# Performance work log

Measured on AMD Instinct MI355X. Metric: run time of the kernel, lower is better.

## Reference

```python
import jax, jax.numpy as jnp
import numpy as np
from jax import lax

B, L, H = 2, 4096, 2048
NH = 16
DK = H // NH  # num_slot = 128 (q/k dim)
C = 64        # chunk size
EPS = 1e-5
N_LAYER = 24


def setup_inputs() -> dict:
    key = jax.random.key(0)
    ks = jax.random.split(key, 7)
    std = 0.02
    return {
        "hidden_states": jax.random.normal(ks[0], (B, L, H), jnp.float32),
        "Wq": jax.random.normal(ks[1], (DK, H), jnp.float32) * std,
        "Wk": jax.random.normal(ks[2], (DK, H), jnp.float32) * std,
        "Wog": jax.random.normal(ks[3], (H, H), jnp.float32) * std,
        "Wig": jax.random.normal(ks[4], (H, H), jnp.float32) * std,
        "Wo": jax.random.normal(ks[5], (H, H), jnp.float32) * (std / np.sqrt(2 * N_LAYER)),
        "g_norm_w": jnp.ones((H,), jnp.float32),
    }


def _gla_chunk(q, k, v, gf):
    # q,k,gf: [b,L,dk]; v: [b,L,dv]. Recurrence: S_t = diag(exp(gf_t)) S_{t-1} + k_t v_t^T; o_t = q_t S_t
    b, Ls, dk = q.shape
    dv = v.shape[-1]
    n = Ls // C
    # [n, b, C, d] so scan iterates over chunks
    qc = q.reshape(b, n, C, dk).transpose(1, 0, 2, 3)
    kc = k.reshape(b, n, C, dk).transpose(1, 0, 2, 3)
    vc = v.reshape(b, n, C, dv).transpose(1, 0, 2, 3)
    gc = gf.reshape(b, n, C, dk).transpose(1, 0, 2, 3)
    Bc = jnp.cumsum(gc, axis=2)  # inclusive within-chunk log-decay

    tril = jnp.tril(jnp.ones((C, C), bool))

    def step(S, inp):
        qh, kh, vh, Bh = inp  # [b,C,dk],[b,C,dk],[b,C,dv],[b,C,dk]
        Blast = Bh[:, -1, :]  # [b,dk]
        # exp(B_i - B_j) <= 1 for j <= i (gf < 0): numerically safe pairwise form
        D = Bh[:, :, None, :] - Bh[:, None, :, :]  # [b,C,C,dk]
        A = jnp.einsum('bid,bjd,bijd->bij', qh, kh, jnp.exp(D))
        A = jnp.where(tril, A, 0.0)
        o_intra = jnp.einsum('bij,bjv->biv', A, vh)
        o_inter = jnp.einsum('bid,bdv->biv', qh * jnp.exp(Bh), S)
        kd = kh * jnp.exp(Blast[:, None, :] - Bh)  # <= 1 scaling, safe
        S_new = S * jnp.exp(Blast)[..., None] + jnp.einsum('bjd,bjv->bdv', kd, vh)
        return S_new, o_intra + o_inter

    S0 = jnp.zeros((b, dk, dv), q.dtype)
    _, o = lax.scan(step, S0, (qc, kc, vc, Bc))  # o: [n,b,C,dv]
    return o.transpose(1, 0, 2, 3).reshape(b, Ls, dv)


def reference(hidden_states, Wq, Wk, Wog, Wig, Wo, g_norm_w):
    x = hidden_states
    q = jax.nn.softmax(x @ Wq.T, axis=-1)        # [b,L,dk]
    k = jax.nn.sigmoid(x @ Wk.T)                 # [b,L,dk]
    v = x                                        # value_dim == hidden_size
    gf = jax.nn.log_sigmoid(-k)                  # per-key-dim log decay, in (-1.32, -0.69)
    o = _gla_chunk(q, k, v, gf)                  # [b,L,H]
    # output gate: og_proj(o) + ig_proj(x), fused RMSNorm + swish gate
    go = o @ Wog.T + x @ Wig.T
    on = o * lax.rsqrt(jnp.mean(o * o, axis=-1, keepdims=True) + EPS) * g_norm_w
    o = on * (go * jax.nn.sigmoid(go))
    return o @ Wo.T
```

## Files before the change

### kernel.cpp

```cpp
#include <hip/hip_runtime.h>
#include <hip/hip_bf16.h>

typedef __hip_bfloat16 bf16;
typedef __bf16 bf16x8 __attribute__((ext_vector_type(8)));
typedef float f32x4 __attribute__((ext_vector_type(4)));

__device__ __forceinline__ void async16(void* lds_base, const void* g) {
  __builtin_amdgcn_global_load_lds(
      (const __attribute__((address_space(1))) void*)g,
      (__attribute__((address_space(3))) void*)lds_base, 16, 0, 0);
}

__global__ void cvt_bf16_kernel(const float* __restrict__ s, bf16* __restrict__ d, int n4) {
  const int i = blockIdx.x * 256 + threadIdx.x;
  if (i >= n4) return;
  const float4 v = ((const float4*)s)[i];
  bf16 h0 = __float2bfloat16(v.x), h1 = __float2bfloat16(v.y);
  bf16 h2 = __float2bfloat16(v.z), h3 = __float2bfloat16(v.w);
  ushort4 o;
  o.x = *(unsigned short*)&h0; o.y = *(unsigned short*)&h1;
  o.z = *(unsigned short*)&h2; o.w = *(unsigned short*)&h3;
  *(ushort4*)((unsigned short*)d + (size_t)i * 4) = o;
}

__global__ void cvt_bf16_strided(const float* __restrict__ s, bf16* __restrict__ d, int n4) {
  const int i = blockIdx.x * 256 + threadIdx.x;
  if (i >= n4) return;
  const int row = i >> 9;
  const int col4 = i & 511;
  const float4 v = ((const float4*)s)[i];
  bf16 h0 = __float2bfloat16(v.x), h1 = __float2bfloat16(v.y);
  bf16 h2 = __float2bfloat16(v.z), h3 = __float2bfloat16(v.w);
  ushort4 o;
  o.x = *(unsigned short*)&h0; o.y = *(unsigned short*)&h1;
  o.z = *(unsigned short*)&h2; o.w = *(unsigned short*)&h3;
  *(ushort4*)((unsigned short*)d + (size_t)row * 4096 + col4 * 4) = o;
}

__global__ __launch_bounds__(256) void convert_x_kernel(
    const float* __restrict__ x, bf16* __restrict__ comb, bf16* __restrict__ xbT) {
  __shared__ float tile[64][65];
  const int b = blockIdx.z;
  const int l0 = blockIdx.x * 64, d0 = blockIdx.y * 64;
  const int t = threadIdx.x;
  const int c4 = (t & 15) * 4, r = t >> 4;
  const size_t base = ((size_t)b * 4096 + l0) * 2048 + d0;
#pragma unroll
  for (int i = 0; i < 4; ++i) {
    const int row = i * 16 + r;
    const float4 v = *(const float4*)(x + base + (size_t)row * 2048 + c4);
    tile[row][c4 + 0] = v.x; tile[row][c4 + 1] = v.y;
    tile[row][c4 + 2] = v.z; tile[row][c4 + 3] = v.w;
    bf16 h0 = __float2bfloat16(v.x), h1 = __float2bfloat16(v.y);
    bf16 h2 = __float2bfloat16(v.z), h3 = __float2bfloat16(v.w);
    ushort4 o;
    o.x = *(unsigned short*)&h0; o.y = *(unsigned short*)&h1;
    o.z = *(unsigned short*)&h2; o.w = *(unsigned short*)&h3;
    *(ushort4*)(comb + ((size_t)(b * 4096 + l0 + row)) * 4096 + 2048 + d0 + c4) = o;
  }
  __syncthreads();
#pragma unroll
  for (int i = 0; i < 4; ++i) {
    const int d = i * 16 + r;
    bf16 h0 = __float2bfloat16(tile[c4 + 0][d]);
    bf16 h1 = __float2bfloat16(tile[c4 + 1][d]);
    bf16 h2 = __float2bfloat16(tile[c4 + 2][d]);
    bf16 h3 = __float2bfloat16(tile[c4 + 3][d]);
    ushort4 o;
    o.x = *(unsigned short*)&h0; o.y = *(unsigned short*)&h1;
    o.z = *(unsigned short*)&h2; o.w = *(unsigned short*)&h3;
    *(ushort4*)(xbT + ((size_t)(b * 2048 + d0 + d)) * 4096 + l0 + c4) = o;
  }
}

__global__ __launch_bounds__(256, 2) void gemm_logits(
    const bf16* __restrict__ A, const bf16* __restrict__ B,
    float* __restrict__ outf, int lda, int N, int K) {
  __shared__ bf16 lA[128 * 32];
  __shared__ bf16 lB[128 * 32];
  const int tid = threadIdx.x;
  const int lane = tid & 63, wave = tid >> 6;
  const int l15 = lane & 15, l4 = lane >> 4;
  const int bm = blockIdx.x * 128, bn = blockIdx.y * 128;
  const int wm = (wave & 1) * 64, wn = (wave >> 1) * 64;
  const int srow = tid >> 2;
  const int skc = (tid & 3) * 8;

  const f32x4 fz = {0.f, 0.f, 0.f, 0.f};
  f32x4 acc[4][4];
#pragma unroll
  for (int i = 0; i < 4; ++i)
#pragma unroll
    for (int j = 0; j < 4; ++j) acc[i][j] = fz;

  bf16* lAu  = lA + wave * 512;
  bf16* lAu2 = lA + 2048 + wave * 512;
  bf16* lBu  = lB + wave * 512;
  bf16* lBu2 = lB + 2048 + wave * 512;

  const bf16* gA0 = A + (size_t)(bm + srow) * lda + skc;
  const bf16* gA1 = A + (size_t)(bm + srow + 64) * lda + skc;
  const bf16* gB0 = B + (size_t)(bn + srow) * K + skc;
  const bf16* gB1 = B + (size_t)(bn + srow + 64) * K + skc;
  for (int k0 = 0; k0 < K; k0 += 32) {
    __syncthreads();
    async16(lAu, gA0 + k0);
    async16(lAu2, gA1 + k0);
    async16(lBu, gB0 + k0);
    async16(lBu2, gB1 + k0);
    __syncthreads();
    bf16x8 af[4], bfv[4];
#pragma unroll
    for (int mt = 0; mt < 4; ++mt)
      af[mt] = *(const bf16x8*)(lA + (wm + mt * 16 + l15) * 32 + l4 * 8);
#pragma unroll
    for (int nt = 0; nt < 4; ++nt)
      bfv[nt] = *(const bf16x8*)(lB + (wn + nt * 16 + l15) * 32 + l4 * 8);
#pragma unroll
    for (int mt = 0; mt < 4; ++mt)
#pragma unroll
      for (int nt = 0; nt < 4; ++nt)
        acc[mt][nt] = __builtin_amdgcn_mfma_f32_16x16x32_bf16(af[mt], bfv[nt], acc[mt][nt], 0, 0, 0);
  }

#pragma unroll
  for (int mt = 0; mt < 4; ++mt)
#pragma unroll
    for (int r = 0; r < 4; ++r) {
      const int gr = bm + wm + mt * 16 + l4 * 4 + r;
#pragma unroll
      for (int nt = 0; nt < 4; ++nt) {
        const int gc = bn + wn + nt * 16 + l15;
        outf[(size_t)gr * N + gc] = acc[mt][nt][r];
      }
    }
}

#define QMFMA(AF, BF, MH, NH)                                               \
  do {                                                                      \
    __builtin_amdgcn_s_setprio(1);                                          \
    _Pragma("unroll") for (int ks_ = 0; ks_ < 2; ++ks_) {                   \
      _Pragma("unroll") for (int mt_ = 0; mt_ < 4; ++mt_) {                 \
        _Pragma("unroll") for (int nt_ = 0; nt_ < 2; ++nt_)                 \
            acc[(MH) * 4 + mt_][(NH) * 2 + nt_] =                           \
                __builtin_amdgcn_mfma_f32_16x16x32_bf16(                    \
                    AF[mt_][ks_], BF[nt_][ks_],                             \
                    acc[(MH) * 4 + mt_][(NH) * 2 + nt_], 0, 0, 0);          \
      }                                                                     \
    }                                                                       \
    __builtin_amdgcn_s_setprio(0);                                          \
  } while (0)

#define READA(AF, PK0, PK1, MH)                                             \
  do {                                                                      \
    _Pragma("unroll") for (int mt_ = 0; mt_ < 4; ++mt_) {                   \
      AF[mt_][0] = *(const bf16x8*)((PK0) + (MH) * 4096 + mt_ * 1024);      \
      AF[mt_][1] = *(const bf16x8*)((PK1) + (MH) * 4096 + mt_ * 1024);      \
    }                                                                       \
  } while (0)

#define READB(BF, PK0, PK1, NH)                                             \
  do {                                                                      \
    _Pragma("unroll") for (int nt_ = 0; nt_ < 2; ++nt_) {                   \
      BF[nt_][0] = *(const bf16x8*)((PK0) + (NH) * 2048 + nt_ * 1024);      \
      BF[nt_][1] = *(const bf16x8*)((PK1) + (NH) * 2048 + nt_ * 1024);      \
    }                                                                       \
  } while (0)

template <int MODE>
__global__ __launch_bounds__(512, 2) void gemm256(
    const bf16* __restrict__ A, const bf16* __restrict__ B,
    float* __restrict__ outf, bf16* __restrict__ outb,
    const bf16* __restrict__ o_in, const float* __restrict__ rmssum,
    const float* __restrict__ gnw, int N, int K, int ostr) {
  __shared__ bf16 lA[2][16384];
  __shared__ bf16 lB[2][16384];
  const int tid = threadIdx.x;
  const int lane = tid & 63;
  const int wave = tid >> 6;
  const int wmi = wave >> 2;
  const int wni = wave & 3;
  const int l15 = lane & 15, l4 = lane >> 4;
  const int axor = l15 & 7;

  const int nwg = gridDim.x;
  const int cpx = nwg >> 3;
  int wg = blockIdx.x;
  wg = (wg & 7) * cpx + (wg >> 3);
  const int NBN = N >> 8;
  const int bm = (wg / NBN) * 256;
  const int bn = (wg % NBN) * 256;

  const int srow = tid >> 3;
  const int scol = ((tid & 7) ^ (srow & 7)) * 8;
  const size_t goff = (size_t)srow * K + scol;
  const int NT = K >> 6;

  const bf16* Ab = A + (size_t)bm * K + goff;
  const bf16* Bb = B + (size_t)bn * K + goff;

  auto stageA = [&](int kt, int h, int buf) {
    const int t = (kt < NT) ? kt : (NT - 1);
    const bf16* g = Ab + (size_t)h * 128 * K + t * 64;
    bf16* d = &lA[buf][h * 8192] + tid * 8;
    async16(d, g);
    async16(d + 4096, g + (size_t)64 * K);
  };
  auto stageB = [&](int kt, int h, int buf) {
    const int t = (kt < NT) ? kt : (NT - 1);
    const bf16* g = Bb + (size_t)h * 128 * K + t * 64;
    bf16* d = &lB[buf][h * 8192] + tid * 8;
    async16(d, g);
    async16(d + 4096, g + (size_t)64 * K);
  };

  const int cK0 = ((l4 ^ (axor & 3)) * 8) + ((axor & 4) ? 32 : 0);
  const int cK1 = ((l4 ^ (axor & 3)) * 8) + ((axor & 4) ? 0 : 32);
  const bf16* pA00 = &lA[0][wmi * 8192 + l15 * 64 + cK0];
  const bf16* pA01 = &lA[0][wmi * 8192 + l15 * 64 + cK1];
  const bf16* pA10 = pA00 + 16384;
  const bf16* pA11 = pA01 + 16384;
  const int bBo = (wni >> 1) * 8192 + ((wni & 1) * 64 + l15) * 64;
  const bf16* pB00 = &lB[0][bBo + cK0];
  const bf16* pB01 = &lB[0][bBo + cK1];
  const bf16* pB10 = pB00 + 16384;
  const bf16* pB11 = pB01 + 16384;

  const f32x4 fz = {0.f, 0.f, 0.f, 0.f};
  f32x4 acc[8][4];
#pragma unroll
  for (int i = 0; i < 8; ++i)
#pragma unroll
    for (int j = 0; j < 4; ++j) acc[i][j] = fz;

  bf16x8 aH0[4][2], aH1[4][2], b0[2][2], b1[2][2];

  stageA(0, 0, 0); stageA(0, 1, 0); stageB(0, 0, 0); stageB(0, 1, 0);
  stageA(1, 0, 1); stageB(1, 0, 1); stageB(1, 1, 1); stageA(1, 1, 1);
  asm volatile("s_waitcnt vmcnt(8)" ::: "memory");
  __builtin_amdgcn_s_barrier();
  READA(aH0, pA00, pA01, 0);
  READB(b0, pB00, pB01, 0);
  __builtin_amdgcn_sched_barrier(0);

  auto ktile = [&](int kt, int cur,
                   const bf16* pAc0, const bf16* pAc1,
                   const bf16* pAn0, const bf16* pAn1,
                   const bf16* pBc0, const bf16* pBc1,
                   const bf16* pBn0, const bf16* pBn1) {
    READB(b1, pBc0, pBc1, 1);
    __builtin_amdgcn_sched_barrier(0);
    asm volatile("s_waitcnt lgkmcnt(4)" ::: "memory");
    __builtin_amdgcn_sched_barrier(0);
    QMFMA(aH0, b0, 0, 0);
    asm volatile("s_waitcnt vmcnt(8)" ::: "memory");
    __builtin_amdgcn_s_barrier();
    READA(aH1, pAc0, pAc1, 1);
    stageA(kt + 2, 0, cur);
    __builtin_amdgcn_sched_barrier(0);
    asm volatile("s_waitcnt lgkmcnt(8)" ::: "memory");
    __builtin_amdgcn_sched_barrier(0);
    QMFMA(aH0, b1, 0, 1);
    asm volatile("s_waitcnt vmcnt(8)" ::: "memory");
    __builtin_amdgcn_s_barrier();
    READA(aH0, pAn0, pAn1, 0);
    stageB(kt + 2, 0, cur);
    stageB(kt + 2, 1, cur);
    __builtin_amdgcn_sched_barrier(0);
    asm volatile("s_waitcnt lgkmcnt(8)" ::: "memory");
    __builtin_amdgcn_sched_barrier(0);
    QMFMA(aH1, b0, 1, 0);
    asm volatile("s_waitcnt vmcnt(10)" ::: "memory");
    __builtin_amdgcn_s_barrier();
    READB(b0, pBn0, pBn1, 0);
    stageA(kt + 2, 1, cur);
    __builtin_amdgcn_sched_barrier(0);
    asm volatile("s_waitcnt lgkmcnt(12)" ::: "memory");
    __builtin_amdgcn_sched_barrier(0);
    QMFMA(aH1, b1, 1, 1);
    asm volatile("s_waitcnt vmcnt(10)" ::: "memory");
    __builtin_amdgcn_s_barrier();
  };

  for (int kt = 0; kt < NT; kt += 2) {
    ktile(kt,     0, pA00, pA01, pA10, pA11, pB00, pB01, pB10, pB11);
    ktile(kt + 1, 1, pA10, pA11, pA00, pA01, pB10, pB11, pB00, pB01);
  }
  asm volatile("s_waitcnt vmcnt(0) lgkmcnt(0)" ::: "memory");
  __builtin_amdgcn_s_barrier();

#pragma unroll
  for (int i = 0; i < 8; ++i) {
#pragma unroll
    for (int r = 0; r < 4; ++r) {
      const int gr = bm + wmi * 128 + i * 16 + l4 * 4 + r;
      float rinv = 0.f;
      if (MODE == 1) rinv = rsqrtf(rmssum[gr] * (1.f / 2048.f) + 1e-5f);
#pragma unroll
      for (int j = 0; j < 4; ++j) {
        const int gc = bn + wni * 64 + j * 16 + l15;
        const float v = acc[i][j][r];
        if (MODE == 1) {
          const float o = (float)o_in[(size_t)gr * ostr + gc];
          const float on = o * rinv * gnw[gc];
          const float sw = v / (1.f + __expf(-v));
          outb[(size_t)gr * N + gc] = __float2bfloat16(on * sw);
        } else {
          outf[(size_t)gr * N + gc] = v;
        }
      }
    }
  }
}

__global__ __launch_bounds__(64) void qk_post_kernel(
    const float* __restrict__ logits, bf16* __restrict__ qb,
    bf16* __restrict__ kb, float* __restrict__ gfl, float* __restrict__ rmssum) {
  const int row = blockIdx.x;
  const int t = threadIdx.x;
  if (t == 0) rmssum[row] = 0.f;
  const float* lr = logits + (size_t)row * 256;
  float a0 = lr[t], a1 = lr[t + 64];
  float m = fmaxf(a0, a1);
#pragma unroll
  for (int s = 32; s; s >>= 1) m = fmaxf(m, __shfl_xor(m, s));
  float e0 = __expf(a0 - m), e1 = __expf(a1 - m);
  float sum = e0 + e1;
#pragma unroll
  for (int s = 32; s; s >>= 1) sum += __shfl_xor(sum, s);
  const float inv = 1.f / sum;
  qb[(size_t)row * 128 + t]      = __float2bfloat16(e0 * inv);
  qb[(size_t)row * 128 + t + 64] = __float2bfloat16(e1 * inv);
  float b0 = lr[128 + t], b1 = lr[128 + t + 64];
  float k0 = 1.f / (1.f + __expf(-b0));
  float k1 = 1.f / (1.f + __expf(-b1));
  kb[(size_t)row * 128 + t]      = __float2bfloat16(k0);
  kb[(size_t)row * 128 + t + 64] = __float2bfloat16(k1);
  gfl[(size_t)row * 128 + t]      = -log1pf(__expf(k0));
  gfl[(size_t)row * 128 + t + 64] = -log1pf(__expf(k1));
}

__global__ __launch_bounds__(256, 2) void gla_kernel(
    const bf16* __restrict__ qb, const bf16* __restrict__ kb,
    const float* __restrict__ gfl, const bf16* __restrict__ xbT,
    bf16* __restrict__ ob, float* __restrict__ rmssum) {
  __shared__ bf16 sF1[64][136];
  __shared__ bf16 sF2[128][136];
  __shared__ float sM[128];
  __shared__ float rowsq[64];
  const int tid = threadIdx.x;
  const int lane = tid & 63, wave = tid >> 6;
  const int l15 = lane & 15, l4 = lane >> 4;
  const int chunk = blockIdx.x, b = blockIdx.y, z = blockIdx.z;
  const int row0 = b * 4096 + chunk * 64;

  if (tid < 64) rowsq[tid] = 0.f;

  if (tid < 128) {
    float s = 0.f;
    for (int i = 0; i <= 32; ++i) s += gfl[(size_t)(row0 + i) * 128 + tid];
    sM[tid] = s;
  }
  __syncthreads();

  if (tid < 128) {
    const int d = tid;
    const float M = sM[d];
    float bi = 0.f;
    for (int i = 0; i < 64; ++i) {
      bi += gfl[(size_t)(row0 + i) * 128 + d];
      const float q = (float)qb[(size_t)(row0 + i) * 128 + d];
      const float k = (float)kb[(size_t)(row0 + i) * 128 + d];
      sF1[i][d]      = __float2bfloat16(q * __expf(bi - M));
      sF2[64 + i][d] = __float2bfloat16(k * __expf(M - bi));
    }
  } else {
    const int d = tid - 128;
    if (chunk == 0) {
      for (int j = 0; j < 64; ++j) sF2[j][d] = __float2bfloat16(0.f);
    } else {
      const float M = sM[d];
      float bw = 0.f;
      for (int j = 63; j >= 0; --j) {
        const float k = (float)kb[(size_t)(row0 - 64 + j) * 128 + d];
        sF2[j][d] = __float2bfloat16(k * __expf(M - bw));
        bw -= gfl[(size_t)(row0 - 64 + j) * 128 + d];
      }
    }
  }
  __syncthreads();

  const f32x4 fz = {0.f, 0.f, 0.f, 0.f};
  {
    f32x4 sacc[4][2];
#pragma unroll
    for (int mt = 0; mt < 4; ++mt) { sacc[mt][0] = fz; sacc[mt][1] = fz; }
    bf16x8 f1[4][4];
#pragma unroll
    for (int kt = 0; kt < 4; ++kt)
#pragma unroll
      for (int mt = 0; mt < 4; ++mt)
        f1[kt][mt] = *(const bf16x8*)(&sF1[mt * 16 + l15][kt * 32 + l4 * 8]);
#pragma unroll
    for (int nt = 0; nt < 2; ++nt)
#pragma unroll
      for (int kt = 0; kt < 4; ++kt) {
        const bf16x8 f2 = *(const bf16x8*)(&sF2[wave * 32 + nt * 16 + l15][kt * 32 + l4 * 8]);
#pragma unroll
        for (int mt = 0; mt < 4; ++mt)
          sacc[mt][nt] = __builtin_amdgcn_mfma_f32_16x16x32_bf16(f1[kt][mt], f2, sacc[mt][nt], 0, 0, 0);
      }
    __syncthreads();
#pragma unroll
    for (int mt = 0; mt < 4; ++mt)
#pragma unroll
      for (int nt = 0; nt < 2; ++nt)
#pragma unroll
        for (int r = 0; r < 4; ++r) {
          const int i = mt * 16 + l4 * 4 + r;
          const int jw = wave * 32 + nt * 16 + l15;
          const bool ok = (jw < 64) || (jw - 64 <= i);
          sF1[i][jw] = __float2bfloat16(ok ? sacc[mt][nt][r] : 0.f);
        }
    __syncthreads();
  }

  bf16x8 av[4][4];
#pragma unroll
  for (int kt = 0; kt < 4; ++kt)
#pragma unroll
    for (int mt = 0; mt < 4; ++mt)
      av[kt][mt] = *(const bf16x8*)(&sF1[mt * 16 + l15][kt * 32 + l4 * 8]);

  float rs[4][4];
#pragma unroll
  for (int a = 0; a < 4; ++a)
#pragma unroll
    for (int r2 = 0; r2 < 4; ++r2) rs[a][r2] = 0.f;

  const int lwb = chunk * 64 - 64;
  for (int dt = z * 4; dt < z * 4 + 4; ++dt) {
    const int c0 = dt * 256 + wave * 64;
    f32x4 oacc[4][4];
#pragma unroll
    for (int mt = 0; mt < 4; ++mt)
#pragma unroll
      for (int nt = 0; nt < 4; ++nt) oacc[mt][nt] = fz;
#pragma unroll
    for (int kt = 0; kt < 4; ++kt)
#pragma unroll
      for (int nt = 0; nt < 4; ++nt) {
        const int dv = c0 + nt * 16 + l15;
        int lw = lwb + kt * 32 + l4 * 8;
        if (lw < 0) lw = 0;
        const bf16x8 vv = *(const bf16x8*)(xbT + ((size_t)b * 2048 + dv) * 4096 + lw);
#pragma unroll
        for (int mt = 0; mt < 4; ++mt)
          oacc[mt][nt] = __builtin_amdgcn_mfma_f32_16x16x32_bf16(av[kt][mt], vv, oacc[mt][nt], 0, 0, 0);
      }
#pragma unroll
    for (int mt = 0; mt < 4; ++mt)
#pragma unroll
      for (int r = 0; r < 4; ++r) {
        const int i = mt * 16 + l4 * 4 + r;
#pragma unroll
        for (int nt = 0; nt < 4; ++nt) {
          const float v = oacc[mt][nt][r];
          ob[(size_t)(row0 + i) * 4096 + (c0 + nt * 16 + l15)] = __float2bfloat16(v);
          rs[mt][r] += v * v;
        }
      }
  }

#pragma unroll
  for (int mt = 0; mt < 4; ++mt)
#pragma unroll
    for (int r = 0; r < 4; ++r) {
      float v = rs[mt][r];
      v += __shfl_xor(v, 1); v += __shfl_xor(v, 2);
      v += __shfl_xor(v, 4); v += __shfl_xor(v, 8);
      if (l15 == 0) atomicAdd(&rowsq[mt * 16 + l4 * 4 + r], v);
    }
  __syncthreads();
  if (tid < 64)
    atomicAdd(&rmssum[row0 + tid], rowsq[tid]);
}

extern "C" void kernel_launch(void* const* d_in, const int* in_sizes, int n_in,
                              void* d_out, int out_size, void* d_ws, size_t ws_size,
                              hipStream_t stream) {
  const float* x   = (const float*)d_in[0];
  const float* Wq  = (const float*)d_in[1];
  const float* Wk  = (const float*)d_in[2];
  const float* Wog = (const float*)d_in[3];
  const float* Wig = (const float*)d_in[4];
  const float* Wo  = (const float*)d_in[5];
  const float* gnw = (const float*)d_in[6];
  float* out = (float*)d_out;

  char* w = (char*)d_ws;
  auto alloc = [&](size_t bytes) {
    char* p = w;
    w += (bytes + 255) & ~(size_t)255;
    return p;
  };
  bf16*  wqkb   = (bf16*)alloc((size_t)256 * 2048 * 2);
  bf16*  wcomb  = (bf16*)alloc((size_t)2048 * 4096 * 2);
  bf16*  wob    = (bf16*)alloc((size_t)2048 * 2048 * 2);
  bf16*  acomb  = (bf16*)alloc((size_t)8192 * 4096 * 2);
  bf16*  xbT    = (bf16*)alloc((size_t)8192 * 2048 * 2);
  float* logits = (float*)alloc((size_t)8192 * 256 * 4);
  bf16*  qbuf   = (bf16*)alloc((size_t)8192 * 128 * 2);
  bf16*  kbuf   = (bf16*)alloc((size_t)8192 * 128 * 2);
  float* gfbuf  = (float*)alloc((size_t)8192 * 128 * 4);
  float* rmsbuf = (float*)alloc((size_t)8192 * 4);
  bf16*  gatedb = xbT;

  cvt_bf16_kernel<<<dim3((65536 + 255) / 256), 256, 0, stream>>>(Wq, wqkb, 65536);
  cvt_bf16_kernel<<<dim3((65536 + 255) / 256), 256, 0, stream>>>(Wk, wqkb + 262144, 65536);
  cvt_bf16_strided<<<dim3((1048576 + 255) / 256), 256, 0, stream>>>(Wog, wcomb, 1048576);
  cvt_bf16_strided<<<dim3((1048576 + 255) / 256), 256, 0, stream>>>(Wig, wcomb + 2048, 1048576);
  cvt_bf16_kernel<<<dim3((1048576 + 255) / 256), 256, 0, stream>>>(Wo, wob, 1048576);

  convert_x_kernel<<<dim3(64, 32, 2), 256, 0, stream>>>(x, acomb, xbT);

  gemm_logits<<<dim3(64, 2), 256, 0, stream>>>(
      acomb + 2048, wqkb, logits, 4096, 256, 2048);

  qk_post_kernel<<<dim3(8192), 64, 0, stream>>>(logits, qbuf, kbuf, gfbuf, rmsbuf);

  gla_kernel<<<dim3(64, 2, 2), 256, 0, stream>>>(qbuf, kbuf, gfbuf, xbT, acomb, rmsbuf);

  gemm256<1><<<dim3(256), 512, 0, stream>>>(
      acomb, wcomb, nullptr, gatedb, acomb, rmsbuf, gnw, 2048, 4096, 4096);

  gemm256<2><<<dim3(256), 512, 0, stream>>>(
      gatedb, wob, out, nullptr, nullptr, nullptr, nullptr, 2048, 2048, 2048);

  (void)in_sizes; (void)n_in; (void)out_size; (void)ws_size;
}
```

Baseline: 436.7 us.

## Split-K the logits GEMM into two halves and reduce in post kernel

The small q/k logits GEMM (8192x256x2048) now runs as a split-K over two K halves via blockIdx.z, doubling the grid from 128 to 256 blocks so more CUs are busy. Each half writes its own fp32 partial buffer, and qk_post_kernel sums the two partials before softmax/sigmoid. qk_post now packs 4 rows per 256-thread block instead of one row per 64-thread block. In gemm256 the prefetch clamp moves out of the stage lambdas into one precomputed offset per k-tile. The split costs an extra fp32 partial buffer, with its write and read traffic.

```diff
diff --git a/kernel.cpp b/kernel.cpp
--- a/kernel.cpp
+++ b/kernel.cpp
@@ -75,16 +75,21 @@
 
 __global__ __launch_bounds__(256, 2) void gemm_logits(
     const bf16* __restrict__ A, const bf16* __restrict__ B,
-    float* __restrict__ outf, int lda, int N, int K) {
+    float* __restrict__ outf, int lda, int ldb, int N, int Kloop) {
   __shared__ bf16 lA[128 * 32];
   __shared__ bf16 lB[128 * 32];
   const int tid = threadIdx.x;
   const int lane = tid & 63, wave = tid >> 6;
   const int l15 = lane & 15, l4 = lane >> 4;
   const int bm = blockIdx.x * 128, bn = blockIdx.y * 128;
+  const int z = blockIdx.z;
   const int wm = (wave & 1) * 64, wn = (wave >> 1) * 64;
   const int srow = tid >> 2;
   const int skc = (tid & 3) * 8;
+
+  A += z * Kloop;
+  B += z * Kloop;
+  outf += (size_t)z * 8192 * 256;
 
   const f32x4 fz = {0.f, 0.f, 0.f, 0.f};
   f32x4 acc[4][4];
@@ -100,9 +105,9 @@
 
   const bf16* gA0 = A + (size_t)(bm + srow) * lda + skc;
   const bf16* gA1 = A + (size_t)(bm + srow + 64) * lda + skc;
-  const bf16* gB0 = B + (size_t)(bn + srow) * K + skc;
-  const bf16* gB1 = B + (size_t)(bn + srow + 64) * K + skc;
-  for (int k0 = 0; k0 < K; k0 += 32) {
+  const bf16* gB0 = B + (size_t)(bn + srow) * ldb + skc;
+  const bf16* gB1 = B + (size_t)(bn + srow + 64) * ldb + skc;
+  for (int k0 = 0; k0 < Kloop; k0 += 32) {
     __syncthreads();
     async16(lAu, gA0 + k0);
     async16(lAu2, gA1 + k0);
@@ -199,16 +204,14 @@
   const bf16* Ab = A + (size_t)bm * K + goff;
   const bf16* Bb = B + (size_t)bn * K + goff;
 
-  auto stageA = [&](int kt, int h, int buf) {
-    const int t = (kt < NT) ? kt : (NT - 1);
-    const bf16* g = Ab + (size_t)h * 128 * K + t * 64;
+  auto stageA = [&](int off, int h, int buf) {
+    const bf16* g = Ab + (size_t)h * 128 * K + off;
     bf16* d = &lA[buf][h * 8192] + tid * 8;
     async16(d, g);
     async16(d + 4096, g + (size_t)64 * K);
   };
-  auto stageB = [&](int kt, int h, int buf) {
-    const int t = (kt < NT) ? kt : (NT - 1);
-    const bf16* g = Bb + (size_t)h * 128 * K + t * 64;
+  auto stageB = [&](int off, int h, int buf) {
+    const bf16* g = Bb + (size_t)h * 128 * K + off;
     bf16* d = &lB[buf][h * 8192] + tid * 8;
     async16(d, g);
     async16(d + 4096, g + (size_t)64 * K);
@@ -236,7 +239,7 @@
   bf16x8 aH0[4][2], aH1[4][2], b0[2][2], b1[2][2];
 
   stageA(0, 0, 0); stageA(0, 1, 0); stageB(0, 0, 0); stageB(0, 1, 0);
-  stageA(1, 0, 1); stageB(1, 0, 1); stageB(1, 1, 1); stageA(1, 1, 1);
+  stageA(64, 0, 1); stageB(64, 0, 1); stageB(64, 1, 1); stageA(64, 1, 1);
   asm volatile("s_waitcnt vmcnt(8)" ::: "memory");
   __builtin_amdgcn_s_barrier();
   READA(aH0, pA00, pA01, 0);
@@ -248,6 +251,7 @@
                    const bf16* pAn0, const bf16* pAn1,
                    const bf16* pBc0, const bf16* pBc1,
                    const bf16* pBn0, const bf16* pBn1) {
+    const int t2 = ((kt + 2 < NT) ? (kt + 2) : (NT - 1)) * 64;
     READB(b1, pBc0, pBc1, 1);
     __builtin_amdgcn_sched_barrier(0);
     asm volatile("s_waitcnt lgkmcnt(4)" ::: "memory");
@@ -256,7 +260,7 @@
     asm volatile("s_waitcnt vmcnt(8)" ::: "memory");
     __builtin_amdgcn_s_barrier();
     READA(aH1, pAc0, pAc1, 1);
-    stageA(kt + 2, 0, cur);
+    stageA(t2, 0, cur);
     __builtin_amdgcn_sched_barrier(0);
     asm volatile("s_waitcnt lgkmcnt(8)" ::: "memory");
     __builtin_amdgcn_sched_barrier(0);
@@ -264,8 +268,8 @@
     asm volatile("s_waitcnt vmcnt(8)" ::: "memory");
     __builtin_amdgcn_s_barrier();
     READA(aH0, pAn0, pAn1, 0);
-    stageB(kt + 2, 0, cur);
-    stageB(kt + 2, 1, cur);
+    stageB(t2, 0, cur);
+    stageB(t2, 1, cur);
     __builtin_amdgcn_sched_barrier(0);
     asm volatile("s_waitcnt lgkmcnt(8)" ::: "memory");
     __builtin_amdgcn_sched_barrier(0);
@@ -273,7 +277,7 @@
     asm volatile("s_waitcnt vmcnt(10)" ::: "memory");
     __builtin_amdgcn_s_barrier();
     READB(b0, pBn0, pBn1, 0);
-    stageA(kt + 2, 1, cur);
+    stageA(t2, 1, cur);
     __builtin_amdgcn_sched_barrier(0);
     asm volatile("s_waitcnt lgkmcnt(12)" ::: "memory");
     __builtin_amdgcn_sched_barrier(0);
@@ -313,14 +317,17 @@
   }
 }
 
-__global__ __launch_bounds__(64) void qk_post_kernel(
-    const float* __restrict__ logits, bf16* __restrict__ qb,
-    bf16* __restrict__ kb, float* __restrict__ gfl, float* __restrict__ rmssum) {
-  const int row = blockIdx.x;
-  const int t = threadIdx.x;
+__global__ __launch_bounds__(256) void qk_post_kernel(
+    const float* __restrict__ l0, const float* __restrict__ l1,
+    bf16* __restrict__ qb, bf16* __restrict__ kb,
+    float* __restrict__ gfl, float* __restrict__ rmssum) {
+  const int t = threadIdx.x & 63;
+  const int row = blockIdx.x * 4 + (threadIdx.x >> 6);
   if (t == 0) rmssum[row] = 0.f;
-  const float* lr = logits + (size_t)row * 256;
-  float a0 = lr[t], a1 = lr[t + 64];
+  const float* lr0 = l0 + (size_t)row * 256;
+  const float* lr1 = l1 + (size_t)row * 256;
+  float a0 = lr0[t] + lr1[t];
+  float a1 = lr0[t + 64] + lr1[t + 64];
   float m = fmaxf(a0, a1);
 #pragma unroll
   for (int s = 32; s; s >>= 1) m = fmaxf(m, __shfl_xor(m, s));
@@ -331,7 +338,8 @@
   const float inv = 1.f / sum;
   qb[(size_t)row * 128 + t]      = __float2bfloat16(e0 * inv);
   qb[(size_t)row * 128 + t + 64] = __float2bfloat16(e1 * inv);
-  float b0 = lr[128 + t], b1 = lr[128 + t + 64];
+  float b0 = lr0[128 + t] + lr1[128 + t];
+  float b1 = lr0[192 + t] + lr1[192 + t];
   float k0 = 1.f / (1.f + __expf(-b0));
   float k1 = 1.f / (1.f + __expf(-b1));
   kb[(size_t)row * 128 + t]      = __float2bfloat16(k0);
@@ -509,7 +517,7 @@
   bf16*  wob    = (bf16*)alloc((size_t)2048 * 2048 * 2);
   bf16*  acomb  = (bf16*)alloc((size_t)8192 * 4096 * 2);
   bf16*  xbT    = (bf16*)alloc((size_t)8192 * 2048 * 2);
-  float* logits = (float*)alloc((size_t)8192 * 256 * 4);
+  float* logits = (float*)alloc((size_t)2 * 8192 * 256 * 4);
   bf16*  qbuf   = (bf16*)alloc((size_t)8192 * 128 * 2);
   bf16*  kbuf   = (bf16*)alloc((size_t)8192 * 128 * 2);
   float* gfbuf  = (float*)alloc((size_t)8192 * 128 * 4);
@@ -524,10 +532,11 @@
 
   convert_x_kernel<<<dim3(64, 32, 2), 256, 0, stream>>>(x, acomb, xbT);
 
-  gemm_logits<<<dim3(64, 2), 256, 0, stream>>>(
-      acomb + 2048, wqkb, logits, 4096, 256, 2048);
-
-  qk_post_kernel<<<dim3(8192), 64, 0, stream>>>(logits, qbuf, kbuf, gfbuf, rmsbuf);
+  gemm_logits<<<dim3(64, 2, 2), 256, 0, stream>>>(
+      acomb + 2048, wqkb, logits, 4096, 2048, 256, 1024);
+
+  qk_post_kernel<<<dim3(2048), 256, 0, stream>>>(
+      logits, logits + (size_t)8192 * 256, qbuf, kbuf, gfbuf, rmsbuf);
 
   gla_kernel<<<dim3(64, 2, 2), 256, 0, stream>>>(qbuf, kbuf, gfbuf, xbT, acomb, rmsbuf);
 
```

Measured after the change: 419.3 us. -4.0%, faster.
